# Kernel tuning notes

Hardware: AMD Instinct MI355X
Metric: run time of the kernel (lower is better)

Reference implementation:

```python
import jax, jax.numpy as jnp
import numpy as np

N_FRAMES = 64
N_ATOMS = 512
SEG_LEN = 1


def get_segments(n_atoms: int, length: int) -> np.ndarray:
    """All ordered pairs of chain segments (i,i+L),(j,j+L) that share no atoms (j-i>L)."""
    starts = np.arange(n_atoms - length)
    i, j = np.meshgrid(starts, starts, indexing='ij')
    mask = (j - i) > length
    i, j = i[mask], j[mask]
    return np.stack([i, i + length, j, j + length], axis=1).astype(np.int32)


def setup_inputs() -> dict:
    key = jax.random.key(0)
    xyz = jax.random.normal(key, (N_FRAMES, N_ATOMS, 3), dtype=jnp.float32)
    segments = jnp.asarray(get_segments(N_ATOMS, SEG_LEN))  # (P, 4) int32
    return {"xyz": xyz, "segments": segments}


def _unit(v):
    return v / jnp.linalg.norm(v, axis=-1, keepdims=True)


def reference(xyz, segments):
    # xyz: (F, N, 3); segments: (P, 4) = [i, i+L, j, j+L]
    p1 = xyz[:, segments[:, 0]]  # (F, P, 3)
    p2 = xyz[:, segments[:, 1]]
    p3 = xyz[:, segments[:, 2]]
    p4 = xyz[:, segments[:, 3]]

    r12 = p2 - p1
    r13 = p3 - p1
    r14 = p4 - p1
    r23 = p3 - p2
    r24 = p4 - p2
    r34 = p4 - p3

    # unit normals of the four faces of the tetrahedron spanned by the segment pair
    n1 = _unit(jnp.cross(r13, r14))
    n2 = _unit(jnp.cross(r14, r24))
    n3 = _unit(jnp.cross(r24, r23))
    n4 = _unit(jnp.cross(r23, r13))

    def asin_dot(a, b):
        return jnp.arcsin(jnp.clip(jnp.sum(a * b, axis=-1), -1.0, 1.0))

    # Gauss linking integral (Klenin & Langowski) per segment pair
    theta = asin_dot(n1, n2) + asin_dot(n2, n3) + asin_dot(n3, n4) + asin_dot(n4, n1)
    sign = jnp.sign(jnp.sum(jnp.cross(r34, r12) * r13, axis=-1))
    wr = theta * sign / (2.0 * jnp.pi)  # (F, P)
    return wr
```

## Files before the change

### kernel.cpp

```cpp
#include <hip/hip_runtime.h>
#include <math.h>

#define NFRAMES 64
#define NATOMS  512
#define NSEG    129795
#define NROWS   509
#define NBLK    255
#define BLOCK   256
#define LDS_SLOTS 576

typedef float v2 __attribute__((ext_vector_type(2)));

__device__ __forceinline__ v2 v2s(float x) { v2 r; r.x = x; r.y = x; return r; }
__device__ __forceinline__ v2 vfma(v2 a, v2 b, v2 c) { return __builtin_elementwise_fma(a, b, c); }
__device__ __forceinline__ v2 vabs(v2 x) { v2 r; r.x = fabsf(x.x); r.y = fabsf(x.y); return r; }
__device__ __forceinline__ v2 vmin1(v2 a) { v2 r; r.x = fminf(a.x, 1.0f); r.y = fminf(a.y, 1.0f); return r; }
__device__ __forceinline__ v2 vsqrt_raw(v2 x) {
    v2 r; r.x = __builtin_amdgcn_sqrtf(x.x); r.y = __builtin_amdgcn_sqrtf(x.y); return r;
}
__device__ __forceinline__ v2 vrsq_raw(v2 x) {
    v2 r; r.x = __builtin_amdgcn_rsqf(x.x); r.y = __builtin_amdgcn_rsqf(x.y); return r;
}
__device__ __forceinline__ v2 vcopysign(v2 m, v2 s) {
    v2 r; r.x = copysignf(m.x, s.x); r.y = copysignf(m.y, s.y); return r;
}

__device__ __forceinline__ v2 vasin(v2 x) {
    v2 ax = vmin1(vabs(x));
    v2 p  = vfma(ax, vfma(ax, vfma(ax, v2s(-0.0187293f), v2s(0.0742610f)), v2s(-0.2121144f)), v2s(1.5707288f));
    v2 r  = v2s(1.57079632679f) - vsqrt_raw(v2s(1.0f) - ax) * p;
    return vcopysign(r, x);
}

struct v23 { v2 x, y, z; };

__device__ __forceinline__ v23 vsub(v23 a, v23 b) { return v23{a.x - b.x, a.y - b.y, a.z - b.z}; }
__device__ __forceinline__ v23 vcross(v23 a, v23 b) {
    return v23{ vfma(a.y, b.z, -(a.z * b.y)),
                vfma(a.z, b.x, -(a.x * b.z)),
                vfma(a.x, b.y, -(a.y * b.x)) };
}
__device__ __forceinline__ v2 vdot(v23 a, v23 b) {
    return vfma(a.x, b.x, vfma(a.y, b.y, a.z * b.z));
}

__device__ __forceinline__ v2 writhe2(const v23& p1, const v23& p2, const v23& p3, const v23& p4) {
    v23 r12 = vsub(p2, p1);
    v23 r13 = vsub(p3, p1);
    v23 r14 = vsub(p4, p1);
    v23 r23 = vsub(p3, p2);
    v23 r24 = vsub(p4, p2);
    v23 r34 = vsub(p4, p3);

    v23 c1 = vcross(r13, r14);
    v23 c2 = vcross(r14, r24);
    v23 c3 = vcross(r24, r23);
    v23 c4 = vcross(r23, r13);

    v2 in1 = vrsq_raw(vdot(c1, c1));
    v2 in2 = vrsq_raw(vdot(c2, c2));
    v2 in3 = vrsq_raw(vdot(c3, c3));
    v2 in4 = vrsq_raw(vdot(c4, c4));

    v2 d12 = vdot(c1, c2) * (in1 * in2);
    v2 d23 = vdot(c2, c3) * (in2 * in3);
    v2 d34 = vdot(c3, c4) * (in3 * in4);
    v2 d41 = vdot(c4, c1) * (in4 * in1);

    v2 theta = (vasin(d12) + vasin(d23)) + (vasin(d34) + vasin(d41));

    v2 sv = vdot(vcross(r34, r12), r13);
    v2 sgn;
    sgn.x = (sv.x > 0.0f) ? 1.0f : ((sv.x < 0.0f) ? -1.0f : 0.0f);
    sgn.y = (sv.y > 0.0f) ? 1.0f : ((sv.y < 0.0f) ? -1.0f : 0.0f);
    return theta * sgn * v2s(0.15915494309189535f);
}

__device__ __forceinline__ int slot_of(int a) { return a + (a >> 3); }

__global__ __launch_bounds__(BLOCK) void writhe_kernel(
    const float* __restrict__ xyz,
    float*       __restrict__ out)
{
    __shared__ float4 sp[LDS_SLOTS];

    const int b = blockIdx.x;
    const int f = blockIdx.y;
    const float* fx = xyz + (size_t)f * (NATOMS * 3);
    for (int a = threadIdx.x; a < NATOMS; a += BLOCK) {
        const float* g = fx + 3 * a;
        sp[slot_of(a)] = make_float4(g[0], g[1], g[2], 0.0f);
    }
    __syncthreads();

    const int rowA = b;
    const int rowB = 508 - b;
    const int lenA = NROWS - rowA;
    const int lenB = (rowB == rowA) ? 0 : NROWS - rowB;
    const int na   = (lenA + 1) >> 1;

    const int t   = threadIdx.x;
    const bool inA = (t < na);
    const int row = inA ? rowA : rowB;
    const int len = inA ? lenA : lenB;
    const int k0  = (inA ? t : (t - na)) << 1;
    if (k0 >= len) return;

    const int j0 = row + 2 + k0;
    float4 A0 = sp[slot_of(j0)];
    float4 A1 = sp[slot_of(j0 + 1)];
    float4 A2 = sp[slot_of(min(j0 + 2, 511))];
    float4 P1 = sp[slot_of(row)];
    float4 P2 = sp[slot_of(row + 1)];

    v23 p1{v2s(P1.x), v2s(P1.y), v2s(P1.z)};
    v23 p2{v2s(P2.x), v2s(P2.y), v2s(P2.z)};
    v23 p3{{A0.x, A1.x}, {A0.y, A1.y}, {A0.z, A1.z}};
    v23 p4{{A1.x, A2.x}, {A1.y, A2.y}, {A1.z, A2.z}};

    v2 w = writhe2(p1, p2, p3, p4);

    const int off = NROWS * row - (row * (row - 1)) / 2;
    const size_t base = (size_t)f * NSEG + off + k0;
    out[base] = w.x;
    if (k0 + 1 < len) out[base + 1] = w.y;
}

extern "C" void kernel_launch(void* const* d_in, const int* in_sizes, int n_in,
                              void* d_out, int out_size, void* d_ws, size_t ws_size,
                              hipStream_t stream) {
    const float* xyz = (const float*)d_in[0];
    float*       out = (float*)d_out;

    dim3 grid(NBLK, NFRAMES);
    writhe_kernel<<<grid, BLOCK, 0, stream>>>(xyz, out);
}
```

Before: 87.94 us.

## Process two frames per block and share difference vectors across the pair

```diff
diff --git a/kernel.cpp b/kernel.cpp
--- a/kernel.cpp
+++ b/kernel.cpp
@@ -7,7 +7,7 @@
 #define NROWS   509
 #define NBLK    255
 #define BLOCK   256
-#define LDS_SLOTS 576
+#define LDS_SLOTS 580
 
 typedef float v2 __attribute__((ext_vector_type(2)));
 
@@ -34,7 +34,6 @@
 
 struct v23 { v2 x, y, z; };
 
-__device__ __forceinline__ v23 vsub(v23 a, v23 b) { return v23{a.x - b.x, a.y - b.y, a.z - b.z}; }
 __device__ __forceinline__ v23 vcross(v23 a, v23 b) {
     return v23{ vfma(a.y, b.z, -(a.z * b.y)),
                 vfma(a.z, b.x, -(a.x * b.z)),
@@ -44,14 +43,8 @@
     return vfma(a.x, b.x, vfma(a.y, b.y, a.z * b.z));
 }
 
-__device__ __forceinline__ v2 writhe2(const v23& p1, const v23& p2, const v23& p3, const v23& p4) {
-    v23 r12 = vsub(p2, p1);
-    v23 r13 = vsub(p3, p1);
-    v23 r14 = vsub(p4, p1);
-    v23 r23 = vsub(p3, p2);
-    v23 r24 = vsub(p4, p2);
-    v23 r34 = vsub(p4, p3);
-
+__device__ __forceinline__ v2 writhe2r(const v23& r12, const v23& r13, const v23& r14,
+                                       const v23& r23, const v23& r24, const v23& r34) {
     v23 c1 = vcross(r13, r14);
     v23 c2 = vcross(r14, r24);
     v23 c3 = vcross(r24, r23);
@@ -82,14 +75,21 @@
     const float* __restrict__ xyz,
     float*       __restrict__ out)
 {
-    __shared__ float4 sp[LDS_SLOTS];
+    __shared__ float4 sp[2][LDS_SLOTS];
 
-    const int b = blockIdx.x;
-    const int f = blockIdx.y;
-    const float* fx = xyz + (size_t)f * (NATOMS * 3);
+    const int b  = blockIdx.x;
+    const int f0 = blockIdx.y * 2;
+    const float* fxa = xyz + (size_t)f0 * (NATOMS * 3);
+    const float* fxb = fxa + NATOMS * 3;
     for (int a = threadIdx.x; a < NATOMS; a += BLOCK) {
-        const float* g = fx + 3 * a;
-        sp[slot_of(a)] = make_float4(g[0], g[1], g[2], 0.0f);
+        const float* g0 = fxa + 3 * a;
+        sp[0][slot_of(a)] = make_float4(g0[0], g0[1], g0[2], 0.0f);
+        const float* g1 = fxb + 3 * a;
+        sp[1][slot_of(a)] = make_float4(g1[0], g1[1], g1[2], 0.0f);
+    }
+    if (threadIdx.x < 2) {
+        sp[0][slot_of(NATOMS + threadIdx.x)] = make_float4(0.f, 0.f, 0.f, 0.f);
+        sp[1][slot_of(NATOMS + threadIdx.x)] = make_float4(0.f, 0.f, 0.f, 0.f);
     }
     __syncthreads();
 
@@ -99,31 +99,49 @@
     const int lenB = (rowB == rowA) ? 0 : NROWS - rowB;
     const int na   = (lenA + 1) >> 1;
 
-    const int t   = threadIdx.x;
+    const int t    = threadIdx.x;
     const bool inA = (t < na);
-    const int row = inA ? rowA : rowB;
-    const int len = inA ? lenA : lenB;
-    const int k0  = (inA ? t : (t - na)) << 1;
+    const int row  = inA ? rowA : rowB;
+    const int len  = inA ? lenA : lenB;
+    const int k0   = (inA ? t : (t - na)) << 1;
     if (k0 >= len) return;
 
-    const int j0 = row + 2 + k0;
-    float4 A0 = sp[slot_of(j0)];
-    float4 A1 = sp[slot_of(j0 + 1)];
-    float4 A2 = sp[slot_of(min(j0 + 2, 511))];
-    float4 P1 = sp[slot_of(row)];
-    float4 P2 = sp[slot_of(row + 1)];
+    const int j0   = row + 2 + k0;
+    const int off  = NROWS * row - (row * (row - 1)) / 2;
+    const size_t base0 = (size_t)f0 * NSEG + off + k0;
+    const bool full = (k0 + 1 < len);
 
-    v23 p1{v2s(P1.x), v2s(P1.y), v2s(P1.z)};
-    v23 p2{v2s(P2.x), v2s(P2.y), v2s(P2.z)};
-    v23 p3{{A0.x, A1.x}, {A0.y, A1.y}, {A0.z, A1.z}};
-    v23 p4{{A1.x, A2.x}, {A1.y, A2.y}, {A1.z, A2.z}};
+    #pragma unroll
+    for (int ff = 0; ff < 2; ++ff) {
+        float4 A0 = sp[ff][slot_of(j0)];
+        float4 A1 = sp[ff][slot_of(j0 + 1)];
+        float4 A2 = sp[ff][slot_of(j0 + 2)];
+        float4 P1 = sp[ff][slot_of(row)];
+        float4 P2 = sp[ff][slot_of(row + 1)];
 
-    v2 w = writhe2(p1, p2, p3, p4);
+        float u0x = A0.x - P1.x, u0y = A0.y - P1.y, u0z = A0.z - P1.z;
+        float u1x = A1.x - P1.x, u1y = A1.y - P1.y, u1z = A1.z - P1.z;
+        float u2x = A2.x - P1.x, u2y = A2.y - P1.y, u2z = A2.z - P1.z;
+        float v0x = A0.x - P2.x, v0y = A0.y - P2.y, v0z = A0.z - P2.z;
+        float v1x = A1.x - P2.x, v1y = A1.y - P2.y, v1z = A1.z - P2.z;
+        float v2x_ = A2.x - P2.x, v2y_ = A2.y - P2.y, v2z_ = A2.z - P2.z;
+        float w0x = A1.x - A0.x, w0y = A1.y - A0.y, w0z = A1.z - A0.z;
+        float w1x = A2.x - A1.x, w1y = A2.y - A1.y, w1z = A2.z - A1.z;
+        float sx  = P2.x - P1.x, sy  = P2.y - P1.y, sz  = P2.z - P1.z;
 
-    const int off = NROWS * row - (row * (row - 1)) / 2;
-    const size_t base = (size_t)f * NSEG + off + k0;
-    out[base] = w.x;
-    if (k0 + 1 < len) out[base + 1] = w.y;
+        v23 r12{{sx, sx}, {sy, sy}, {sz, sz}};
+        v23 r13{{u0x, u1x}, {u0y, u1y}, {u0z, u1z}};
+        v23 r14{{u1x, u2x}, {u1y, u2y}, {u1z, u2z}};
+        v23 r23{{v0x, v1x}, {v0y, v1y}, {v0z, v1z}};
+        v23 r24{{v1x, v2x_}, {v1y, v2y_}, {v1z, v2z_}};
+        v23 r34{{w0x, w1x}, {w0y, w1y}, {w0z, w1z}};
+
+        v2 w = writhe2r(r12, r13, r14, r23, r24, r34);
+
+        const size_t base = base0 + (size_t)ff * NSEG;
+        out[base] = w.x;
+        if (full) out[base + 1] = w.y;
+    }
 }
 
 extern "C" void kernel_launch(void* const* d_in, const int* in_sizes, int n_in,
@@ -132,6 +150,6 @@
     const float* xyz = (const float*)d_in[0];
     float*       out = (float*)d_out;
 
-    dim3 grid(NBLK, NFRAMES);
+    dim3 grid(NBLK, NFRAMES / 2);
     writhe_kernel<<<grid, BLOCK, 0, stream>>>(xyz, out);
 }
```

Result: no change. 86.73 us (-1.4%).
